# Kernel tuning notes

Hardware: AMD Instinct MI355X
Metric: run time of the kernel (lower is better)

Reference implementation:

```python
import jax, jax.numpy as jnp
import numpy as np

N_NODES = 100000
N_EDGES = 1600000
K = 10          # APPNP propagation steps
ALPHA = 0.1     # teleport probability


def appnp_propagate(src, dst, h):
    """DGL APPNPConv (eval mode, no edge dropout): symmetric-normalized
    k-step personalized-pagerank propagation over the edge list."""
    n = h.shape[0]
    deg = jax.ops.segment_sum(jnp.ones_like(dst, dtype=h.dtype), dst, num_segments=n)
    norm = jnp.clip(deg, 1.0, None) ** -0.5  # [N]
    h0 = h
    for _ in range(K):
        msg = (h * norm[:, None])[src]                      # [E, D] gather
        agg = jax.ops.segment_sum(msg, dst, num_segments=n) # [N, D] scatter-add
        h = (1.0 - ALPHA) * agg * norm[:, None] + ALPHA * h0
    return h


def setup_inputs() -> dict:
    key = jax.random.key(0)
    ks = jax.random.split(key, 7)
    input_dim, hidden, classes = 256, 48, 16
    features = jax.random.normal(ks[0], (N_NODES, input_dim), dtype=jnp.float32)
    src = jax.random.randint(ks[1], (N_EDGES,), 0, N_NODES, dtype=jnp.int32)
    dst = jax.random.randint(ks[2], (N_EDGES,), 0, N_NODES, dtype=jnp.int32)
    # xavier_normal-ish init for fc weights
    W1 = jax.random.normal(ks[3], (hidden, input_dim), dtype=jnp.float32) * (2.0 / (hidden + input_dim)) ** 0.5
    b1 = jnp.zeros((hidden,), dtype=jnp.float32)
    W2 = jax.random.normal(ks[4], (classes, hidden), dtype=jnp.float32) * (2.0 / (classes + hidden)) ** 0.5
    b2 = jnp.zeros((classes,), dtype=jnp.float32)
    return {"features": features, "src": src, "dst": dst,
            "W1": W1, "b1": b1, "W2": W2, "b2": b2}


def reference(features, src, dst, W1, b1, W2, b2):
    # fc1
    h = features @ W1.T + b1              # [N, hidden]
    # layer1: APPNP propagation
    x = appnp_propagate(src, dst, h)
    # fc2 + elu
    x = jax.nn.elu(x @ W2.T + b2)         # [N, classes]
    # layer2: APPNP propagation
    x = appnp_propagate(src, dst, x)
    return jax.nn.elu(x)
```

## Files before the change

kernel.cpp:

```cpp
#include <hip/hip_runtime.h>
#include <hip/hip_fp16.h>
#include <math.h>

#define IN_DIM 256
#define HID 48
#define CLS 16
#define K_STEPS 10
#define ALPHA 0.1f


__global__ void zero_int_kernel(int* __restrict__ p, int n) {
    int i = blockIdx.x * blockDim.x + threadIdx.x;
    if (i < n) p[i] = 0;
}

__global__ void hist_kernel(const int* __restrict__ dst, int* __restrict__ deg, int nE) {
    int i = blockIdx.x * blockDim.x + threadIdx.x;
    if (i < nE) atomicAdd(&deg[dst[i]], 1);
}

__global__ void norm_kernel(const int* __restrict__ deg, float* __restrict__ nrm, int n) {
    int i = blockIdx.x * blockDim.x + threadIdx.x;
    if (i < n) nrm[i] = rsqrtf(fmaxf((float)deg[i], 1.0f));
}


__global__ __launch_bounds__(256) void scan1_kernel(const int* __restrict__ deg,
                                                    int* __restrict__ bsum, int n) {
    __shared__ int ls[256];
    int t = threadIdx.x;
    int base = blockIdx.x * 1024 + t * 4;
    int s = 0;
    if (base + 3 < n) {
        int4 d = *(const int4*)(deg + base);
        s = d.x + d.y + d.z + d.w;
    } else {
        for (int i = 0; i < 4; i++) if (base + i < n) s += deg[base + i];
    }
    ls[t] = s; __syncthreads();
    for (int o = 128; o > 0; o >>= 1) {
        if (t < o) ls[t] += ls[t + o];
        __syncthreads();
    }
    if (t == 0) bsum[blockIdx.x] = ls[0];
}

__global__ void scan2_kernel(int* __restrict__ bsum, int* __restrict__ off, int nb, int n) {
    if (threadIdx.x == 0 && blockIdx.x == 0) {
        int run = 0;
        for (int i = 0; i < nb; i++) { int t = bsum[i]; bsum[i] = run; run += t; }
        off[n] = run;
    }
}

__global__ __launch_bounds__(256) void scan3_kernel(const int* __restrict__ deg,
                                                    const int* __restrict__ bsum,
                                                    int* __restrict__ off,
                                                    int* __restrict__ cursor, int n) {
    __shared__ int ts[256];
    int t = threadIdx.x;
    int base = blockIdx.x * 1024 + t * 4;
    int d0 = 0, d1 = 0, d2 = 0, d3 = 0;
    if (base + 3 < n) {
        int4 d = *(const int4*)(deg + base);
        d0 = d.x; d1 = d.y; d2 = d.z; d3 = d.w;
    } else {
        if (base     < n) d0 = deg[base];
        if (base + 1 < n) d1 = deg[base + 1];
        if (base + 2 < n) d2 = deg[base + 2];
        if (base + 3 < n) d3 = deg[base + 3];
    }
    int s = d0 + d1 + d2 + d3;
    ts[t] = s; __syncthreads();
    for (int o = 1; o < 256; o <<= 1) {
        int v = (t >= o) ? ts[t - o] : 0;
        __syncthreads();
        ts[t] += v;
        __syncthreads();
    }
    int ex = ts[t] - s + bsum[blockIdx.x];
    int p0 = ex, p1 = ex + d0, p2 = p1 + d1, p3 = p2 + d2;
    if (base     < n) { off[base]     = p0; cursor[base]     = p0; }
    if (base + 1 < n) { off[base + 1] = p1; cursor[base + 1] = p1; }
    if (base + 2 < n) { off[base + 2] = p2; cursor[base + 2] = p2; }
    if (base + 3 < n) { off[base + 3] = p3; cursor[base + 3] = p3; }
}

__global__ void fill_kernel(const int* __restrict__ src, const int* __restrict__ dst,
                            int* __restrict__ cursor, int* __restrict__ csrc, int nE) {
    int e = blockIdx.x * blockDim.x + threadIdx.x;
    if (e >= nE) return;
    int p = atomicAdd(&cursor[dst[e]], 1);
    csrc[p] = src[e];
}


__global__ __launch_bounds__(256) void wc_kernel(
    const float* __restrict__ W1, const float* __restrict__ W2,
    const float* __restrict__ b1, float* __restrict__ Wc, float* __restrict__ bc)
{
    int c = blockIdx.x;
    int k = threadIdx.x;
    float acc = 0.0f;
    #pragma unroll
    for (int j = 0; j < HID; j++)
        acc = fmaf(W2[c * HID + j], W1[j * IN_DIM + k], acc);
    Wc[c * IN_DIM + k] = acc;
    if (k == 0) {
        float b = 0.0f;
        for (int j = 0; j < HID; j++) b = fmaf(W2[c * HID + j], b1[j], b);
        bc[c] = b;
    }
}


#define BM 128
#define BK 16
__global__ __launch_bounds__(256) void fcz_kernel(
    const float* __restrict__ X, const float* __restrict__ Wc,
    const float* __restrict__ bc, const float* __restrict__ nrm,
    float* __restrict__ z0, __half* __restrict__ A, int n)
{
    __shared__ float Xs[BK][BM + 1];
    __shared__ float Ws[BK][CLS];
    const int t = threadIdx.x;
    const int tx = t & 31;
    const int ty = t >> 5;
    const int mbase = blockIdx.x * BM;
    float acc[4][2] = {{0}};

    for (int k0 = 0; k0 < IN_DIM; k0 += BK) {
        #pragma unroll
        for (int c0 = 0; c0 < 2; c0++) {
            int c = t + c0 * 256;
            int m = c >> 2, kc = (c & 3) << 2;
            int gm = mbase + m;
            float4 xv = make_float4(0.f, 0.f, 0.f, 0.f);
            if (gm < n) xv = *(const float4*)(X + (size_t)gm * IN_DIM + k0 + kc);
            Xs[kc + 0][m] = xv.x; Xs[kc + 1][m] = xv.y;
            Xs[kc + 2][m] = xv.z; Xs[kc + 3][m] = xv.w;
        }
        if (t < 64) {
            int j = t >> 2, kc = (t & 3) << 2;
            float4 wv = *(const float4*)(Wc + (size_t)j * IN_DIM + k0 + kc);
            Ws[kc + 0][j] = wv.x; Ws[kc + 1][j] = wv.y;
            Ws[kc + 2][j] = wv.z; Ws[kc + 3][j] = wv.w;
        }
        __syncthreads();
        #pragma unroll
        for (int k = 0; k < BK; k++) {
            float a[4], b[2];
            #pragma unroll
            for (int im = 0; im < 4; im++) a[im] = Xs[k][tx + 32 * im];
            #pragma unroll
            for (int jn = 0; jn < 2; jn++) b[jn] = Ws[k][ty * 2 + jn];
            #pragma unroll
            for (int im = 0; im < 4; im++)
                #pragma unroll
                for (int jn = 0; jn < 2; jn++)
                    acc[im][jn] = fmaf(a[im], b[jn], acc[im][jn]);
        }
        __syncthreads();
    }

    #pragma unroll
    for (int im = 0; im < 4; im++) {
        int m = mbase + tx + 32 * im;
        if (m < n) {
            float nv = nrm[m];
            float r0 = acc[im][0] + bc[ty * 2 + 0];
            float r1 = acc[im][1] + bc[ty * 2 + 1];
            size_t idx = (size_t)m * CLS + ty * 2;
            z0[idx] = r0;
            z0[idx + 1] = r1;
            ((__half2*)A)[(size_t)m * 8 + ty] = __floats2half2_rn(r0 * nv, r1 * nv);
        }
    }
}


struct __align__(8) half4 { __half2 a, b; };

__device__ __forceinline__ void hacc(float4& acc, half4 w) {
    float2 lo = __half22float2(w.a);
    float2 hi = __half22float2(w.b);
    acc.x += lo.x; acc.y += lo.y; acc.z += hi.x; acc.w += hi.y;
}
__device__ __forceinline__ float eluf(float x) {
    return x > 0.0f ? x : expm1f(x);
}

template<int MODE>
__global__ __launch_bounds__(256) void gatherh_kernel(
    const int* __restrict__ off, const int* __restrict__ csrc,
    const half4* __restrict__ A, const float4* __restrict__ tele,
    const float* __restrict__ nrm, const float4* __restrict__ b2v,
    half4* __restrict__ outp, float4* __restrict__ x0out,
    float4* __restrict__ outf, int n)
{
    const int v = blockIdx.x * 64 + threadIdx.y;
    if (v >= n) return;
    const int lane = threadIdx.x;

    const int s = off[v], e = off[v + 1];
    float4 a0 = make_float4(0.f, 0.f, 0.f, 0.f), a1 = a0;
    int i = s;
    for (; i + 3 < e; i += 4) {
        int u0 = csrc[i], u1 = csrc[i + 1], u2 = csrc[i + 2], u3 = csrc[i + 3];
        half4 w0 = A[(size_t)u0 * 4 + lane];
        half4 w1 = A[(size_t)u1 * 4 + lane];
        half4 w2 = A[(size_t)u2 * 4 + lane];
        half4 w3 = A[(size_t)u3 * 4 + lane];
        hacc(a0, w0); hacc(a1, w1); hacc(a0, w2); hacc(a1, w3);
    }
    for (; i < e; i++) hacc(a0, A[(size_t)csrc[i] * 4 + lane]);
    a0.x += a1.x; a0.y += a1.y; a0.z += a1.z; a0.w += a1.w;

    float nv = nrm[v];
    size_t o = (size_t)v * 4 + lane;
    float4 hv = tele[o];
    float4 r;
    r.x = (1.0f - ALPHA) * a0.x * nv + ALPHA * hv.x;
    r.y = (1.0f - ALPHA) * a0.y * nv + ALPHA * hv.y;
    r.z = (1.0f - ALPHA) * a0.z * nv + ALPHA * hv.z;
    r.w = (1.0f - ALPHA) * a0.w * nv + ALPHA * hv.w;

    if (MODE == 0) {
        half4 w;
        w.a = __floats2half2_rn(r.x * nv, r.y * nv);
        w.b = __floats2half2_rn(r.z * nv, r.w * nv);
        outp[o] = w;
    } else if (MODE == 1) {
        float4 b = b2v[lane];
        float4 x;
        x.x = eluf(r.x + b.x); x.y = eluf(r.y + b.y);
        x.z = eluf(r.z + b.z); x.w = eluf(r.w + b.w);
        x0out[o] = x;
        half4 w;
        w.a = __floats2half2_rn(x.x * nv, x.y * nv);
        w.b = __floats2half2_rn(x.z * nv, x.w * nv);
        outp[o] = w;
    } else {
        outf[o] = make_float4(eluf(r.x), eluf(r.y), eluf(r.z), eluf(r.w));
    }
}


extern "C" void kernel_launch(void* const* d_in, const int* in_sizes, int n_in,
                              void* d_out, int out_size, void* d_ws, size_t ws_size,
                              hipStream_t stream)
{
    const float* features = (const float*)d_in[0];
    const int*   src      = (const int*)d_in[1];
    const int*   dst      = (const int*)d_in[2];
    const float* W1       = (const float*)d_in[3];
    const float* b1       = (const float*)d_in[4];
    const float* W2       = (const float*)d_in[5];
    const float* b2       = (const float*)d_in[6];
    float* out = (float*)d_out;

    const int n  = in_sizes[0] / IN_DIM;
    const int nE = in_sizes[1];

    float* ws   = (float*)d_ws;
    float* nrm  = ws;
    float* z0   = nrm + n;
    float* x0   = z0 + (size_t)CLS * n;
    float* Wc   = x0 + (size_t)CLS * n;
    float* bc   = Wc + CLS * IN_DIM;
    __half* PH  = (__half*)(bc + 16);
    __half* QH  = PH + (size_t)CLS * n;
    int*   deg    = (int*)(QH + (size_t)CLS * n);
    int*   off    = deg + n;
    int*   cursor = off + n + 4;
    int*   bsum   = cursor + n;
    int*   csrc   = bsum + 1024;

    const int B = 256;
    const int nb = (n + 1023) / 1024;

    zero_int_kernel<<<(n + B - 1) / B, B, 0, stream>>>(deg, n);
    hist_kernel<<<(nE + B - 1) / B, B, 0, stream>>>(dst, deg, nE);
    norm_kernel<<<(n + B - 1) / B, B, 0, stream>>>(deg, nrm, n);
    scan1_kernel<<<nb, 256, 0, stream>>>(deg, bsum, n);
    scan2_kernel<<<1, 64, 0, stream>>>(bsum, off, nb, n);
    scan3_kernel<<<nb, 256, 0, stream>>>(deg, bsum, off, cursor, n);
    fill_kernel<<<(nE + B - 1) / B, B, 0, stream>>>(src, dst, cursor, csrc, nE);

    wc_kernel<<<CLS, 256, 0, stream>>>(W1, W2, b1, Wc, bc);
    fcz_kernel<<<(n + BM - 1) / BM, 256, 0, stream>>>(features, Wc, bc, nrm, z0, PH, n);

    dim3 gblk(4, 64);
    int ggrid = (n + 63) / 64;

    __half* pa = PH; __half* pb = QH;
    for (int k = 0; k < K_STEPS; k++) {
        if (k < K_STEPS - 1)
            gatherh_kernel<0><<<ggrid, gblk, 0, stream>>>(
                off, csrc, (const half4*)pa, (const float4*)z0, nrm,
                nullptr, (half4*)pb, nullptr, nullptr, n);
        else
            gatherh_kernel<1><<<ggrid, gblk, 0, stream>>>(
                off, csrc, (const half4*)pa, (const float4*)z0, nrm,
                (const float4*)b2, (half4*)pb, (float4*)x0, nullptr, n);
        __half* t = pa; pa = pb; pb = t;
    }

    for (int k = 0; k < K_STEPS; k++) {
        if (k < K_STEPS - 1)
            gatherh_kernel<0><<<ggrid, gblk, 0, stream>>>(
                off, csrc, (const half4*)pa, (const float4*)x0, nrm,
                nullptr, (half4*)pb, nullptr, nullptr, n);
        else
            gatherh_kernel<2><<<ggrid, gblk, 0, stream>>>(
                off, csrc, (const half4*)pa, (const float4*)x0, nrm,
                nullptr, nullptr, nullptr, (float4*)out, n);
        __half* t = pa; pa = pb; pb = t;
    }
}
```

Baseline: 610.6 us.

## Partition CSR fill by destination range per XCD and vectorize index loads

The CSR fill kernel now splits destinations into 8 ranges, keyed by blockIdx.x & 7. Each group of blocks scans all edges but only handles destinations in its own range, so the atomics and csrc writes for a range come from blocks likely placed on the same XCD and stay in that chiplet's L2. The cost is that every group reads the whole dst array, eight reads in total. Separately, the gather loop now aligns its start and loads four neighbor indices at once as an int4, which cuts the number of index load instructions.

```diff
diff --git a/kernel.cpp b/kernel.cpp
--- a/kernel.cpp
+++ b/kernel.cpp
@@ -86,12 +86,22 @@
     if (base + 3 < n) { off[base + 3] = p3; cursor[base + 3] = p3; }
 }
 
-__global__ void fill_kernel(const int* __restrict__ src, const int* __restrict__ dst,
-                            int* __restrict__ cursor, int* __restrict__ csrc, int nE) {
-    int e = blockIdx.x * blockDim.x + threadIdx.x;
-    if (e >= nE) return;
-    int p = atomicAdd(&cursor[dst[e]], 1);
-    csrc[p] = src[e];
+
+__global__ __launch_bounds__(256) void fill8_kernel(
+    const int* __restrict__ src, const int* __restrict__ dst,
+    int* __restrict__ cursor, int* __restrict__ csrc, int nE, int nper)
+{
+    const int g  = blockIdx.x & 7;
+    const int bi = blockIdx.x >> 3;
+    const int nb = gridDim.x >> 3;
+    const int lo = g * nper, hi = lo + nper;
+    for (int i = bi * 256 + threadIdx.x; i < nE; i += nb * 256) {
+        int d = dst[i];
+        if (d >= lo && d < hi) {
+            int p = atomicAdd(&cursor[d], 1);
+            csrc[p] = src[i];
+        }
+    }
 }
 
 
@@ -205,12 +215,14 @@
     const int s = off[v], e = off[v + 1];
     float4 a0 = make_float4(0.f, 0.f, 0.f, 0.f), a1 = a0;
     int i = s;
-    for (; i + 3 < e; i += 4) {
-        int u0 = csrc[i], u1 = csrc[i + 1], u2 = csrc[i + 2], u3 = csrc[i + 3];
-        half4 w0 = A[(size_t)u0 * 4 + lane];
-        half4 w1 = A[(size_t)u1 * 4 + lane];
-        half4 w2 = A[(size_t)u2 * 4 + lane];
-        half4 w3 = A[(size_t)u3 * 4 + lane];
+    for (; i < e && (i & 3); i++)
+        hacc(a0, A[(size_t)csrc[i] * 4 + lane]);
+    for (; i + 4 <= e; i += 4) {
+        int4 u = *(const int4*)(csrc + i);
+        half4 w0 = A[(size_t)u.x * 4 + lane];
+        half4 w1 = A[(size_t)u.y * 4 + lane];
+        half4 w2 = A[(size_t)u.z * 4 + lane];
+        half4 w3 = A[(size_t)u.w * 4 + lane];
         hacc(a0, w0); hacc(a1, w1); hacc(a0, w2); hacc(a1, w3);
     }
     for (; i < e; i++) hacc(a0, A[(size_t)csrc[i] * 4 + lane]);
@@ -278,6 +290,7 @@
 
     const int B = 256;
     const int nb = (n + 1023) / 1024;
+    const int nper = (n + 7) / 8;
 
     zero_int_kernel<<<(n + B - 1) / B, B, 0, stream>>>(deg, n);
     hist_kernel<<<(nE + B - 1) / B, B, 0, stream>>>(dst, deg, nE);
@@ -285,7 +298,8 @@
     scan1_kernel<<<nb, 256, 0, stream>>>(deg, bsum, n);
     scan2_kernel<<<1, 64, 0, stream>>>(bsum, off, nb, n);
     scan3_kernel<<<nb, 256, 0, stream>>>(deg, bsum, off, cursor, n);
-    fill_kernel<<<(nE + B - 1) / B, B, 0, stream>>>(src, dst, cursor, csrc, nE);
+
+    fill8_kernel<<<2048, 256, 0, stream>>>(src, dst, cursor, csrc, nE, nper);
 
     wc_kernel<<<CLS, 256, 0, stream>>>(W1, W2, b1, Wc, bc);
     fcz_kernel<<<(n + BM - 1) / BM, 256, 0, stream>>>(features, Wc, bc, nrm, z0, PH, n);
```

Measured after the change: 565.3 us. 1.08x faster.
